# Performance work log

Measured on AMD Instinct MI355X. Metric: run time of the kernel, lower is better.

The kernel has to match this reference:

```python
import jax, jax.numpy as jnp
import numpy as np
from jax import lax

HIDDEN = 512
EPS = 1e-5


def _conv(x, w):
    # NCHW conv, 3x3, SAME padding, no bias (padding = kernel_size // 2 == 1)
    return lax.conv_general_dilated(
        x, w, window_strides=(1, 1), padding='SAME',
        dimension_numbers=('NCHW', 'OIHW', 'NCHW'))


def setup_inputs() -> dict:
    key = jax.random.key(0)
    ks = jax.random.split(key, 5)
    N, C, H, W = 32, HIDDEN, 32, 32
    fan = C * 9
    std = float(1.0 / np.sqrt(fan))
    return {
        'x': jax.random.normal(ks[0], (N, C, H, W), jnp.float32),
        'w_q': jax.random.normal(ks[1], (C, C, 3, 3), jnp.float32) * std,
        'w_k': jax.random.normal(ks[2], (C, C, 3, 3), jnp.float32) * std,
        'w_v': jax.random.normal(ks[3], (C, C, 3, 3), jnp.float32) * std,
        'w_o': jax.random.normal(ks[4], (C, C, 3, 3), jnp.float32) * std,
        'gamma': jnp.ones((C,), jnp.float32),
        'beta': jnp.zeros((C,), jnp.float32),
    }


def reference(x, w_q, w_k, w_v, w_o, gamma, beta):
    C = x.shape[1]
    q = _conv(x, w_q)  # [N,C,H,W]
    k = _conv(x, w_k)
    v = _conv(x, w_v)
    # (query.unsqueeze(1) * key.unsqueeze(0)).sum(2) == channel contraction
    att = jnp.einsum('ichw,jchw->ijhw', q, k) / jnp.sqrt(jnp.asarray(C, x.dtype))
    att = jax.nn.softmax(att, axis=1)  # softmax over key instances
    virt = jnp.einsum('ijhw,jchw->ichw', att, v)  # [N,C,H,W]
    # GroupNorm(1, C): normalize over (C,H,W) per instance, per-channel affine
    mean = jnp.mean(virt, axis=(1, 2, 3), keepdims=True)
    var = jnp.var(virt, axis=(1, 2, 3), keepdims=True)
    virt = (virt - mean) * lax.rsqrt(var + EPS)
    virt = virt * gamma[None, :, None, None] + beta[None, :, None, None]
    virt = jax.nn.relu(virt)
    virt = _conv(virt, w_o)
    # Dropout(0.2) is identity in eval mode
    return x + virt
```

## Files before the change

kernel.cpp:

```cpp
#include <hip/hip_runtime.h>

namespace {

constexpr int kN  = 32;
constexpr int kC  = 512;
constexpr int kH  = 32;
constexpr int kW  = 32;
constexpr int kHW = kH * kW;

constexpr int PCH   = 36992;
constexpr size_t WTF_ELEMS = (size_t)9 * kC * kC;
constexpr size_t XH_ELEMS  = (size_t)kN * 16 * PCH;
constexpr size_t QKV_ELEMS = (size_t)kN * kHW * kC;

using bf16x8 = __attribute__((ext_vector_type(8))) short;
using bf16x4 = __attribute__((ext_vector_type(4))) short;
using f32x4  = __attribute__((ext_vector_type(4))) float;

__device__ __forceinline__ float bf2f(short s) {
  unsigned u = ((unsigned)(unsigned short)s) << 16;
  return __builtin_bit_cast(float, u);
}
__device__ __forceinline__ short f2bf(float f) {
  unsigned u = __builtin_bit_cast(unsigned, f);
  u += 0x7FFFu + ((u >> 16) & 1u);
  return (short)(u >> 16);
}
__device__ __forceinline__ void gload_lds16(const void* g, void* l) {
  __builtin_amdgcn_global_load_lds(
      (const __attribute__((address_space(1))) void*)g,
      (__attribute__((address_space(3))) void*)l, 16, 0, 0);
}

__global__ __launch_bounds__(256) void wtf_pack_kernel(
    const float* __restrict__ wq, const float* __restrict__ wk,
    const float* __restrict__ wv, const float* __restrict__ wo,
    short* __restrict__ oq, short* __restrict__ ok,
    short* __restrict__ ov, short* __restrict__ oo) {
  const float* wsrc[4] = {wq, wk, wv, wo};
  short* wdst[4] = {oq, ok, ov, oo};
  const float* w = wsrc[blockIdx.z];
  short* wtf = wdst[blockIdx.z];
  __shared__ float tile[32][289];
  const int co0 = blockIdx.x * 32;
  const int ci0 = blockIdx.y * 32;
  for (int idx = threadIdx.x; idx < 32 * 288; idx += 256) {
    int c = idx % 288, r = idx / 288;
    tile[r][c] = w[(size_t)(co0 + r) * (kC * 9) + (size_t)ci0 * 9 + c];
  }
  __syncthreads();
  const int kkb  = ci0 >> 5;
  const int nnG0 = co0 >> 4;
  for (int g = threadIdx.x; g < 9 * 2 * 64; g += 256) {
    int laneg = g & 63;
    int nnL   = (g >> 6) & 1;
    int t     = g >> 7;
    int hi    = laneg >> 4;
    int coL   = nnL * 16 + (laneg & 15);
    bf16x8 pk;
#pragma unroll
    for (int j = 0; j < 8; ++j) pk[j] = f2bf(tile[coL][(hi * 8 + j) * 9 + t]);
    *(bf16x8*)&wtf[(((size_t)t * 16 + kkb) * 32 + nnG0 + nnL) * 512 + laneg * 8] = pk;
  }
}

__global__ __launch_bounds__(256) void x2xh_kernel(
    const float* __restrict__ x, short* __restrict__ xh) {
  __shared__ float tile[32][33];
  const int ch = blockIdx.x;
  const int h  = blockIdx.y;
  const int n  = blockIdx.z;
  const int w0 = threadIdx.x & 31;
  const int c0 = threadIdx.x >> 5;
#pragma unroll
  for (int pass = 0; pass < 4; ++pass) {
    int cir = pass * 8 + c0;
    tile[w0][cir] = x[(((size_t)n * kC + ch * 32 + cir) * kH + h) * kW + w0];
  }
  __syncthreads();
  const int wv = threadIdx.x >> 3;
  const int g4 = (threadIdx.x & 7) * 4;
  bf16x4 pk;
#pragma unroll
  for (int j = 0; j < 4; ++j) pk[j] = f2bf(tile[wv][g4 + j]);
  *(bf16x4*)&xh[(((size_t)n * 16 + ch) * 1156 + (size_t)(h + 1) * 34 + (wv + 1)) * 32 + g4] = pk;
}

__global__ __launch_bounds__(256) void halo_zero_kernel(
    short* __restrict__ xh, short* __restrict__ vh) {
  short* base = (blockIdx.x & 1) ? vh : xh;
  const int plane = blockIdx.x >> 1;
  short* dst = base + (size_t)plane * PCH;
  const int t = threadIdx.x;
  if (t < 132) {
    int row, col;
    if (t < 34)       { row = 0;          col = t; }
    else if (t < 68)  { row = 33;         col = t - 34; }
    else if (t < 100) { row = t - 68 + 1; col = 0; }
    else              { row = t - 100 + 1; col = 33; }
    const bf16x8 z = {0, 0, 0, 0, 0, 0, 0, 0};
    short* q = dst + (size_t)(row * 34 + col) * 32;
#pragma unroll
    for (int j = 0; j < 4; ++j) *(bf16x8*)&q[j * 8] = z;
  }
}

__global__ __launch_bounds__(256, 3) void conv_qkv_kernel(
    const short* __restrict__ xin,
    const short* __restrict__ wtq, const short* __restrict__ wtk,
    const short* __restrict__ wtv,
    short* __restrict__ outq, short* __restrict__ outk,
    short* __restrict__ outv) {
  __shared__ __align__(16) short As[3][8192];
  const int tid  = threadIdx.x;
  const int lane = tid & 63;
  const int l15  = lane & 15, lhi = lane >> 4;
  const int w    = tid >> 6;
  const int wbase = tid & 192;

  const int xcd = blockIdx.x & 7;
  const int m   = blockIdx.x >> 3;
  const int co0 = (m >> 5) * 64;
  const int spt = m & 7;
  const int n   = xcd * 4 + ((m >> 3) & 3);
  const int h0  = spt * 4;
  const int sp0 = spt * 128;

  const short* srcA = xin + (size_t)n * (16 * PCH) + (size_t)h0 * (34 * 32);
  const size_t boff = ((size_t)(co0 >> 4) + w) * 512 + lane * 8;
  const short* bp[3] = {wtq + boff, wtk + boff, wtv + boff};

  f32x4 acc[3][8];
#pragma unroll
  for (int c = 0; c < 3; ++c)
#pragma unroll
    for (int mf = 0; mf < 8; ++mf)
#pragma unroll
      for (int r = 0; r < 4; ++r) acc[c][mf][r] = 0.f;

#define STAGE_A(kk, buf)                                                      \
  {                                                                           \
    const short* gA = srcA + (size_t)(kk) * PCH;                              \
    _Pragma("unroll") for (int pass = 0; pass < 4; ++pass)                    \
        gload_lds16(gA + (size_t)(pass * 256 + tid) * 8,                      \
                    &As[buf][(pass * 256 + wbase) * 8]);                      \
  }

  STAGE_A(0, 0);
  STAGE_A(1, 1);
  bf16x8 cur[3];
#pragma unroll
  for (int j = 0; j < 3; ++j)
    cur[j] = *(const bf16x8*)&bp[j][0];

  int ab = 0;
  int sb = 2;
  for (int kk = 0; kk < 16; ++kk) {
    asm volatile("s_waitcnt vmcnt(7)" ::: "memory");
    __builtin_amdgcn_s_barrier();
#pragma unroll
    for (int t = 0; t < 9; ++t) {
      if (t == 1 && kk < 14) STAGE_A(kk + 2, sb);
      const int dy = t / 3, dx = t % 3;
      bf16x8 a[8];
#pragma unroll
      for (int mf = 0; mf < 8; ++mf) {
        const int pb = ((mf >> 1) + dy) * 34 + (mf & 1) * 16 + l15 + dx;
        a[mf] = *(const bf16x8*)&As[ab][pb * 32 + lhi * 8];
      }
      const int nt  = (t < 8) ? (t + 1) : 0;
      const int nkk = (t < 8) ? kk : kk + 1;
      const size_t bo = (size_t)(nt * 16 + nkk) * 16384;
#pragma unroll
      for (int c = 0; c < 3; ++c) {
        __builtin_amdgcn_s_setprio(1);
#pragma unroll
        for (int mf = 0; mf < 8; ++mf)
          acc[c][mf] = __builtin_amdgcn_mfma_f32_16x16x32_bf16(
              a[mf], cur[c], acc[c][mf], 0, 0, 0);
        __builtin_amdgcn_s_setprio(0);
        cur[c] = *(const bf16x8*)&bp[c][bo];
      }
    }
    ab = (ab == 2) ? 0 : ab + 1;
    sb = (sb == 2) ? 0 : sb + 1;
  }
#undef STAGE_A

  short* outs[3] = {outq, outk, outv};
#pragma unroll
  for (int c = 0; c < 3; ++c) {
    short* out = outs[c];
#pragma unroll
    for (int mf = 0; mf < 8; ++mf)
#pragma unroll
      for (int r = 0; r < 4; ++r) {
        size_t off = ((size_t)n * kHW + sp0 + mf * 16 + lhi * 4 + r) * kC
                     + co0 + w * 16 + l15;
        out[off] = f2bf(acc[c][mf][r]);
      }
  }
}

__global__ __launch_bounds__(256, 3) void conv_o_kernel(
    const short* __restrict__ xin, const short* __restrict__ wtf,
    const float* __restrict__ xres, float* __restrict__ out) {
  __shared__ __align__(16) short As[3][8192];
  const int tid  = threadIdx.x;
  const int lane = tid & 63;
  const int l15  = lane & 15, lhi = lane >> 4;
  const int w    = tid >> 6;
  const int wbase = tid & 192;

  const int xcd = blockIdx.x & 7;
  const int m   = blockIdx.x >> 3;
  const int co0 = (m >> 5) * 128;
  const int spt = m & 7;
  const int n   = xcd * 4 + ((m >> 3) & 3);
  const int h0  = spt * 4;
  const int sp0 = spt * 128;

  const short* srcA = xin + (size_t)n * (16 * PCH) + (size_t)h0 * (34 * 32);
  const short* bptr = wtf + ((size_t)(co0 >> 4) + w * 2) * 512 + lane * 8;

  f32x4 acc[2][8];
#pragma unroll
  for (int nf = 0; nf < 2; ++nf)
#pragma unroll
    for (int mf = 0; mf < 8; ++mf)
#pragma unroll
      for (int r = 0; r < 4; ++r) acc[nf][mf][r] = 0.f;

#define STAGE_A(kk, buf)                                                      \
  {                                                                           \
    const short* gA = srcA + (size_t)(kk) * PCH;                              \
    _Pragma("unroll") for (int pass = 0; pass < 4; ++pass)                    \
        gload_lds16(gA + (size_t)(pass * 256 + tid) * 8,                      \
                    &As[buf][(pass * 256 + wbase) * 8]);                      \
  }

  STAGE_A(0, 0);
  STAGE_A(1, 1);
  bf16x8 cur[2], nxt[2];
#pragma unroll
  for (int j = 0; j < 2; ++j)
    cur[j] = *(const bf16x8*)&bptr[(size_t)j * 512];

  int ab = 0, sb = 2;
  for (int kk = 0; kk < 16; ++kk) {
    asm volatile("s_waitcnt vmcnt(6)" ::: "memory");
    __builtin_amdgcn_s_barrier();
#pragma unroll
    for (int t = 0; t < 9; ++t) {
      {
        const int nt  = (t < 8) ? (t + 1) : 0;
        const int nkk = (t < 8) ? kk : kk + 1;
        const size_t bo = (size_t)(nt * 16 + nkk) * 16384;
#pragma unroll
        for (int j = 0; j < 2; ++j)
          nxt[j] = *(const bf16x8*)&bptr[bo + (size_t)j * 512];
      }
      if (t == 1 && kk < 14) STAGE_A(kk + 2, sb);
      const int dy = t / 3, dx = t % 3;
      bf16x8 a[8];
#pragma unroll
      for (int mf = 0; mf < 8; ++mf) {
        const int pb = ((mf >> 1) + dy) * 34 + (mf & 1) * 16 + l15 + dx;
        a[mf] = *(const bf16x8*)&As[ab][pb * 32 + lhi * 8];
      }
      __builtin_amdgcn_s_setprio(1);
#pragma unroll
      for (int nf = 0; nf < 2; ++nf)
#pragma unroll
        for (int mf = 0; mf < 8; ++mf)
          acc[nf][mf] = __builtin_amdgcn_mfma_f32_16x16x32_bf16(
              a[mf], cur[nf], acc[nf][mf], 0, 0, 0);
      __builtin_amdgcn_s_setprio(0);
#pragma unroll
      for (int j = 0; j < 2; ++j) cur[j] = nxt[j];
    }
    ab = (ab == 2) ? 0 : ab + 1;
    sb = (sb == 2) ? 0 : sb + 1;
  }
#undef STAGE_A

  float* T = (float*)&As[0][0];
#pragma unroll
  for (int nf = 0; nf < 2; ++nf) {
    __syncthreads();
    const int tr = w * 16 + l15;
#pragma unroll
    for (int mf = 0; mf < 8; ++mf)
#pragma unroll
      for (int r = 0; r < 4; ++r)
        T[tr * 129 + mf * 16 + lhi * 4 + r] = acc[nf][mf][r];
    __syncthreads();
#pragma unroll
    for (int it = 0; it < 32; ++it) {
      int idx = it * 256 + tid;
      int trr = idx >> 7, sp = idx & 127;
      int co = co0 + (trr >> 4) * 32 + nf * 16 + (trr & 15);
      size_t off = ((size_t)n * kC + co) * kHW + sp0 + sp;
      out[off] = T[trr * 129 + sp] + xres[off];
    }
  }
}

__global__ __launch_bounds__(256) void attn_mfma_kernel(
    const short* q, const short* __restrict__ k,
    const short* __restrict__ v, short* virt, float* __restrict__ gsum) {
  __shared__ __align__(16) short Qs[32 * 72];
  __shared__ __align__(16) short Ks[32 * 72];
  __shared__ __align__(16) float Ps[32 * 36];
  __shared__ __align__(16) short Vt[64 * 40];
  const int p    = blockIdx.x;
  const int tid  = threadIdx.x;
  const int lane = tid & 63;
  const int l15  = lane & 15, lhi = lane >> 4;
  const int w    = tid >> 6;
  const int iq   = w >> 1, jq = w & 1;

  f32x4 accS = {0.f, 0.f, 0.f, 0.f};
  const int si = tid >> 3;
  const int sc = (tid & 7) * 8;
  for (int c0 = 0; c0 < kC; c0 += 64) {
    __syncthreads();
    {
      size_t g = ((size_t)si * kHW + p) * kC + c0 + sc;
      *(bf16x8*)&Qs[si * 72 + sc] = *(const bf16x8*)&q[g];
      *(bf16x8*)&Ks[si * 72 + sc] = *(const bf16x8*)&k[g];
    }
    __syncthreads();
#pragma unroll
    for (int cs = 0; cs < 2; ++cs) {
      bf16x8 aq = *(const bf16x8*)&Qs[(iq * 16 + l15) * 72 + cs * 32 + lhi * 8];
      bf16x8 bk = *(const bf16x8*)&Ks[(jq * 16 + l15) * 72 + cs * 32 + lhi * 8];
      accS = __builtin_amdgcn_mfma_f32_16x16x32_bf16(aq, bk, accS, 0, 0, 0);
    }
  }
  __syncthreads();
  constexpr float scale = 0.044194173824159216f;
#pragma unroll
  for (int r = 0; r < 4; ++r)
    Ps[(iq * 16 + lhi * 4 + r) * 36 + jq * 16 + l15] = accS[r] * scale;
  __syncthreads();

  {
    const int i  = tid >> 3;
    const int j0 = (tid & 7) * 4;
    float a0 = Ps[i * 36 + j0], a1 = Ps[i * 36 + j0 + 1];
    float a2 = Ps[i * 36 + j0 + 2], a3 = Ps[i * 36 + j0 + 3];
    float mx = fmaxf(fmaxf(a0, a1), fmaxf(a2, a3));
    for (int off = 1; off < 8; off <<= 1) mx = fmaxf(mx, __shfl_xor(mx, off));
    float e0 = __expf(a0 - mx), e1 = __expf(a1 - mx);
    float e2 = __expf(a2 - mx), e3 = __expf(a3 - mx);
    float s = e0 + e1 + e2 + e3;
    for (int off = 1; off < 8; off <<= 1) s += __shfl_xor(s, off);
    const float inv = 1.f / s;
    Ps[i * 36 + j0]     = e0 * inv;
    Ps[i * 36 + j0 + 1] = e1 * inv;
    Ps[i * 36 + j0 + 2] = e2 * inv;
    Ps[i * 36 + j0 + 3] = e3 * inv;
  }
  __syncthreads();

  bf16x8 ap[2];
#pragma unroll
  for (int it = 0; it < 2; ++it) {
    const float* pr = &Ps[(it * 16 + l15) * 36 + lhi * 8];
    float4 lo = *(const float4*)pr;
    float4 hi4 = *(const float4*)(pr + 4);
    ap[it][0] = f2bf(lo.x);  ap[it][1] = f2bf(lo.y);
    ap[it][2] = f2bf(lo.z);  ap[it][3] = f2bf(lo.w);
    ap[it][4] = f2bf(hi4.x); ap[it][5] = f2bf(hi4.y);
    ap[it][6] = f2bf(hi4.z); ap[it][7] = f2bf(hi4.w);
  }
  __syncthreads();

  float gs[8], gq2[8];
#pragma unroll
  for (int idx = 0; idx < 8; ++idx) { gs[idx] = 0.f; gq2[idx] = 0.f; }

  const f32x4 zacc = {0.f, 0.f, 0.f, 0.f};
  for (int c0 = 0; c0 < kC; c0 += 64) {
    __syncthreads();
    {
      const int j = tid >> 3, c8g = tid & 7;
      bf16x8 vvv = *(const bf16x8*)&v[((size_t)j * kHW + p) * kC + c0 + c8g * 8];
#pragma unroll
      for (int jj = 0; jj < 8; ++jj) {
        int c = c8g * 8 + jj;
        int byte = (c * 80 + j * 2) ^ (((c >> 3) & 7) << 4);
        *(short*)((char*)Vt + byte) = vvv[jj];
      }
    }
    __syncthreads();
    {
      const int c = w * 16 + l15;
      const int byte = (c * 80 + lhi * 16) ^ (((c >> 3) & 7) << 4);
      bf16x8 bv = *(const bf16x8*)((const char*)Vt + byte);
#pragma unroll
      for (int it = 0; it < 2; ++it) {
        f32x4 o = __builtin_amdgcn_mfma_f32_16x16x32_bf16(ap[it], bv, zacc, 0, 0, 0);
#pragma unroll
        for (int r = 0; r < 4; ++r) {
          short ob = f2bf(o[r]);
          virt[((size_t)(it * 16 + lhi * 4 + r) * kHW + p) * kC + c0 + w * 16 + l15] = ob;
          float fv = bf2f(ob);
          gs[it * 4 + r] += fv;
          gq2[it * 4 + r] = fmaf(fv, fv, gq2[it * 4 + r]);
        }
      }
    }
  }

#pragma unroll
  for (int idx = 0; idx < 8; ++idx)
    for (int off = 1; off < 16; off <<= 1) {
      gs[idx]  += __shfl_xor(gs[idx], off);
      gq2[idx] += __shfl_xor(gq2[idx], off);
    }
  __syncthreads();
  float* SS = Ps;
  if (l15 == 0) {
#pragma unroll
    for (int idx = 0; idx < 8; ++idx) {
      int it = idx >> 2, r = idx & 3;
      int i = it * 16 + lhi * 4 + r;
      SS[(w * 32 + i) * 2]     = gs[idx];
      SS[(w * 32 + i) * 2 + 1] = gq2[idx];
    }
  }
  __syncthreads();
  if (tid < 32) {
    float s = 0.f, q2 = 0.f;
#pragma unroll
    for (int ww = 0; ww < 4; ++ww) {
      s  += SS[(ww * 32 + tid) * 2];
      q2 += SS[(ww * 32 + tid) * 2 + 1];
    }
    atomicAdd(&gsum[tid], s);
    atomicAdd(&gsum[32 + tid], q2);
  }
}

__global__ __launch_bounds__(64) void gn_final_kernel(
    const float* __restrict__ gsum, float* __restrict__ stats) {
  if (threadIdx.x < 32) {
    constexpr float invn = 1.f / ((float)kHW * kC);
    float mean = gsum[threadIdx.x] * invn;
    float var = gsum[32 + threadIdx.x] * invn - mean * mean;
    stats[threadIdx.x] = mean;
    stats[32 + threadIdx.x] = rsqrtf(var + 1e-5f);
  }
}

__global__ __launch_bounds__(256) void gn_apply_kernel(
    const short* __restrict__ virt, const float* __restrict__ stats,
    const float* __restrict__ gamma, const float* __restrict__ beta,
    short* __restrict__ vh) {
  const size_t g = (size_t)blockIdx.x * 256 + threadIdx.x;
  const int i    = (int)(g >> 16);
  const int rest = (int)(g & 65535);
  const int p    = rest >> 6;
  const int c8g  = rest & 63;
  const int ci   = c8g * 8;
  const float mean = stats[i];
  const float rstd = stats[32 + i];
  bf16x8 vv = *(const bf16x8*)&virt[((size_t)i * kHW + p) * kC + ci];
  const float4 ga = ((const float4*)gamma)[c8g * 2];
  const float4 gb = ((const float4*)gamma)[c8g * 2 + 1];
  const float4 ba = ((const float4*)beta)[c8g * 2];
  const float4 bb = ((const float4*)beta)[c8g * 2 + 1];
  const float gv[8] = {ga.x, ga.y, ga.z, ga.w, gb.x, gb.y, gb.z, gb.w};
  const float bv[8] = {ba.x, ba.y, ba.z, ba.w, bb.x, bb.y, bb.z, bb.w};
  bf16x8 o;
#pragma unroll
  for (int jj = 0; jj < 8; ++jj) {
    float f = (bf2f(vv[jj]) - mean) * rstd;
    f = fmaxf(fmaf(f, gv[jj], bv[jj]), 0.f);
    o[jj] = f2bf(f);
  }
  const size_t dst =
      (((size_t)i * 16 + (ci >> 5)) * 1156 + (size_t)((p >> 5) + 1) * 34 + (p & 31) + 1) * 32
      + (ci & 31);
  *(bf16x8*)&vh[dst] = o;
}

}

extern "C" void kernel_launch(void* const* d_in, const int* in_sizes, int n_in,
                              void* d_out, int out_size, void* d_ws,
                              size_t ws_size, hipStream_t stream) {
  const float* x     = (const float*)d_in[0];
  const float* w_q   = (const float*)d_in[1];
  const float* w_k   = (const float*)d_in[2];
  const float* w_v   = (const float*)d_in[3];
  const float* w_o   = (const float*)d_in[4];
  const float* gamma = (const float*)d_in[5];
  const float* beta  = (const float*)d_in[6];

  short* ws    = (short*)d_ws;
  short* wtf_q = ws;
  short* wtf_k = wtf_q + WTF_ELEMS;
  short* wtf_v = wtf_k + WTF_ELEMS;
  short* wtf_o = wtf_v + WTF_ELEMS;
  short* xh    = wtf_o + WTF_ELEMS;
  short* vh    = xh + XH_ELEMS;
  short* qb    = vh + XH_ELEMS;
  short* kb    = qb + QKV_ELEMS;
  short* vb    = kb + QKV_ELEMS;
  float* stats = (float*)(vb + QKV_ELEMS);
  float* gsum  = stats + 64;
  short* virt  = qb;
  halo_zero_kernel<<<1024, 256, 0, stream>>>(xh, vh);
  hipMemsetAsync(gsum, 0, 64 * sizeof(float), stream);

  wtf_pack_kernel<<<dim3(16, 16, 4), 256, 0, stream>>>(
      w_q, w_k, w_v, w_o, wtf_q, wtf_k, wtf_v, wtf_o);

  x2xh_kernel<<<dim3(16, 32, 32), 256, 0, stream>>>(x, xh);

  conv_qkv_kernel<<<2048, 256, 0, stream>>>(xh, wtf_q, wtf_k, wtf_v,
                                            qb, kb, vb);

  attn_mfma_kernel<<<kHW, 256, 0, stream>>>(qb, kb, vb, virt, gsum);

  gn_final_kernel<<<1, 64, 0, stream>>>(gsum, stats);
  gn_apply_kernel<<<(int)(QKV_ELEMS / 8 / 256), 256, 0, stream>>>(
      virt, stats, gamma, beta, vh);

  conv_o_kernel<<<1024, 256, 0, stream>>>(vh, wtf_o, x, (float*)d_out);
}
```

Measured before the change: 553.3 us.

## Interleave QKV weights and double-buffer attention LDS tiles with register prefetch

The packed Q/K/V conv weights now sit interleaved in one buffer, so each wave's three weight fragments for a tap are adjacent in memory and come from one base pointer, which should improve locality and reduce address arithmetic. The attention kernel double-buffers its Q/K and V LDS tiles and prefetches the next channel slice into registers while the current slice is consumed. This removes one barrier per loop iteration and hides global load latency, at the cost of extra LDS and register use.

```diff
diff --git a/kernel.cpp b/kernel.cpp
--- a/kernel.cpp
+++ b/kernel.cpp
@@ -35,12 +35,10 @@
 __global__ __launch_bounds__(256) void wtf_pack_kernel(
     const float* __restrict__ wq, const float* __restrict__ wk,
     const float* __restrict__ wv, const float* __restrict__ wo,
-    short* __restrict__ oq, short* __restrict__ ok,
-    short* __restrict__ ov, short* __restrict__ oo) {
+    short* __restrict__ wqkv, short* __restrict__ wo_out) {
   const float* wsrc[4] = {wq, wk, wv, wo};
-  short* wdst[4] = {oq, ok, ov, oo};
-  const float* w = wsrc[blockIdx.z];
-  short* wtf = wdst[blockIdx.z];
+  const int z = blockIdx.z;
+  const float* w = wsrc[z];
   __shared__ float tile[32][289];
   const int co0 = blockIdx.x * 32;
   const int ci0 = blockIdx.y * 32;
@@ -60,7 +58,13 @@
     bf16x8 pk;
 #pragma unroll
     for (int j = 0; j < 8; ++j) pk[j] = f2bf(tile[coL][(hi * 8 + j) * 9 + t]);
-    *(bf16x8*)&wtf[(((size_t)t * 16 + kkb) * 32 + nnG0 + nnL) * 512 + laneg * 8] = pk;
+    if (z < 3) {
+      *(bf16x8*)&wqkv[((((size_t)t * 16 + kkb) * 32 + nnG0 + nnL) * 3 + z) * 512
+                      + laneg * 8] = pk;
+    } else {
+      *(bf16x8*)&wo_out[(((size_t)t * 16 + kkb) * 32 + nnG0 + nnL) * 512
+                        + laneg * 8] = pk;
+    }
   }
 }
 
@@ -106,9 +110,7 @@
 }
 
 __global__ __launch_bounds__(256, 3) void conv_qkv_kernel(
-    const short* __restrict__ xin,
-    const short* __restrict__ wtq, const short* __restrict__ wtk,
-    const short* __restrict__ wtv,
+    const short* __restrict__ xin, const short* __restrict__ wqkv,
     short* __restrict__ outq, short* __restrict__ outk,
     short* __restrict__ outv) {
   __shared__ __align__(16) short As[3][8192];
@@ -127,8 +129,7 @@
   const int sp0 = spt * 128;
 
   const short* srcA = xin + (size_t)n * (16 * PCH) + (size_t)h0 * (34 * 32);
-  const size_t boff = ((size_t)(co0 >> 4) + w) * 512 + lane * 8;
-  const short* bp[3] = {wtq + boff, wtk + boff, wtv + boff};
+  const short* bbase = wqkv + ((size_t)(co0 >> 4) + w) * 1536 + lane * 8;
 
   f32x4 acc[3][8];
 #pragma unroll
@@ -151,7 +152,7 @@
   bf16x8 cur[3];
 #pragma unroll
   for (int j = 0; j < 3; ++j)
-    cur[j] = *(const bf16x8*)&bp[j][0];
+    cur[j] = *(const bf16x8*)&bbase[(size_t)j * 512];
 
   int ab = 0;
   int sb = 2;
@@ -170,7 +171,8 @@
       }
       const int nt  = (t < 8) ? (t + 1) : 0;
       const int nkk = (t < 8) ? kk : kk + 1;
-      const size_t bo = (size_t)(nt * 16 + nkk) * 16384;
+      const size_t bo = (size_t)(nt * 16 + nkk) * 49152;
+      const short* brel = &bbase[bo];
 #pragma unroll
       for (int c = 0; c < 3; ++c) {
         __builtin_amdgcn_s_setprio(1);
@@ -179,7 +181,7 @@
           acc[c][mf] = __builtin_amdgcn_mfma_f32_16x16x32_bf16(
               a[mf], cur[c], acc[c][mf], 0, 0, 0);
         __builtin_amdgcn_s_setprio(0);
-        cur[c] = *(const bf16x8*)&bp[c][bo];
+        cur[c] = *(const bf16x8*)&brel[(size_t)c * 512];
       }
     }
     ab = (ab == 2) ? 0 : ab + 1;
@@ -309,10 +311,10 @@
 __global__ __launch_bounds__(256) void attn_mfma_kernel(
     const short* q, const short* __restrict__ k,
     const short* __restrict__ v, short* virt, float* __restrict__ gsum) {
-  __shared__ __align__(16) short Qs[32 * 72];
-  __shared__ __align__(16) short Ks[32 * 72];
+  __shared__ __align__(16) short Qs[2][32 * 72];
+  __shared__ __align__(16) short Ks[2][32 * 72];
   __shared__ __align__(16) float Ps[32 * 36];
-  __shared__ __align__(16) short Vt[64 * 40];
+  __shared__ __align__(16) short Vt[2][64 * 40];
   const int p    = blockIdx.x;
   const int tid  = threadIdx.x;
   const int lane = tid & 63;
@@ -323,18 +325,22 @@
   f32x4 accS = {0.f, 0.f, 0.f, 0.f};
   const int si = tid >> 3;
   const int sc = (tid & 7) * 8;
-  for (int c0 = 0; c0 < kC; c0 += 64) {
+  const size_t gstep = ((size_t)si * kHW + p) * kC + sc;
+  bf16x8 rq = *(const bf16x8*)&q[gstep];
+  bf16x8 rk = *(const bf16x8*)&k[gstep];
+  for (int i = 0; i < 8; ++i) {
+    const int cb = i & 1;
+    *(bf16x8*)&Qs[cb][si * 72 + sc] = rq;
+    *(bf16x8*)&Ks[cb][si * 72 + sc] = rk;
+    if (i < 7) {
+      rq = *(const bf16x8*)&q[gstep + (i + 1) * 64];
+      rk = *(const bf16x8*)&k[gstep + (i + 1) * 64];
+    }
     __syncthreads();
-    {
-      size_t g = ((size_t)si * kHW + p) * kC + c0 + sc;
-      *(bf16x8*)&Qs[si * 72 + sc] = *(const bf16x8*)&q[g];
-      *(bf16x8*)&Ks[si * 72 + sc] = *(const bf16x8*)&k[g];
-    }
-    __syncthreads();
 #pragma unroll
     for (int cs = 0; cs < 2; ++cs) {
-      bf16x8 aq = *(const bf16x8*)&Qs[(iq * 16 + l15) * 72 + cs * 32 + lhi * 8];
-      bf16x8 bk = *(const bf16x8*)&Ks[(jq * 16 + l15) * 72 + cs * 32 + lhi * 8];
+      bf16x8 aq = *(const bf16x8*)&Qs[cb][(iq * 16 + l15) * 72 + cs * 32 + lhi * 8];
+      bf16x8 bk = *(const bf16x8*)&Ks[cb][(jq * 16 + l15) * 72 + cs * 32 + lhi * 8];
       accS = __builtin_amdgcn_mfma_f32_16x16x32_bf16(aq, bk, accS, 0, 0, 0);
     }
   }
@@ -382,23 +388,27 @@
   for (int idx = 0; idx < 8; ++idx) { gs[idx] = 0.f; gq2[idx] = 0.f; }
 
   const f32x4 zacc = {0.f, 0.f, 0.f, 0.f};
-  for (int c0 = 0; c0 < kC; c0 += 64) {
+  const int vj = tid >> 3, vc8 = tid & 7;
+  const size_t vstep = ((size_t)vj * kHW + p) * kC + vc8 * 8;
+  bf16x8 rv = *(const bf16x8*)&v[vstep];
+  for (int i = 0; i < 8; ++i) {
+    const int cb = i & 1;
+    {
+      char* vtb = (char*)&Vt[cb][0];
+#pragma unroll
+      for (int jj = 0; jj < 8; ++jj) {
+        int c = vc8 * 8 + jj;
+        int byte = (c * 80 + vj * 2) ^ (((c >> 3) & 7) << 4);
+        *(short*)(vtb + byte) = rv[jj];
+      }
+    }
+    if (i < 7) rv = *(const bf16x8*)&v[vstep + (i + 1) * 64];
     __syncthreads();
     {
-      const int j = tid >> 3, c8g = tid & 7;
-      bf16x8 vvv = *(const bf16x8*)&v[((size_t)j * kHW + p) * kC + c0 + c8g * 8];
-#pragma unroll
-      for (int jj = 0; jj < 8; ++jj) {
-        int c = c8g * 8 + jj;
-        int byte = (c * 80 + j * 2) ^ (((c >> 3) & 7) << 4);
-        *(short*)((char*)Vt + byte) = vvv[jj];
-      }
-    }
-    __syncthreads();
-    {
+      const int c0 = i * 64;
       const int c = w * 16 + l15;
       const int byte = (c * 80 + lhi * 16) ^ (((c >> 3) & 7) << 4);
-      bf16x8 bv = *(const bf16x8*)((const char*)Vt + byte);
+      bf16x8 bv = *(const bf16x8*)((const char*)&Vt[cb][0] + byte);
 #pragma unroll
       for (int it = 0; it < 2; ++it) {
         f32x4 o = __builtin_amdgcn_mfma_f32_16x16x32_bf16(ap[it], bv, zacc, 0, 0, 0);
@@ -501,10 +511,8 @@
   const float* beta  = (const float*)d_in[6];
 
   short* ws    = (short*)d_ws;
-  short* wtf_q = ws;
-  short* wtf_k = wtf_q + WTF_ELEMS;
-  short* wtf_v = wtf_k + WTF_ELEMS;
-  short* wtf_o = wtf_v + WTF_ELEMS;
+  short* wqkv  = ws;
+  short* wtf_o = wqkv + 3 * WTF_ELEMS;
   short* xh    = wtf_o + WTF_ELEMS;
   short* vh    = xh + XH_ELEMS;
   short* qb    = vh + XH_ELEMS;
@@ -517,12 +525,11 @@
   hipMemsetAsync(gsum, 0, 64 * sizeof(float), stream);
 
   wtf_pack_kernel<<<dim3(16, 16, 4), 256, 0, stream>>>(
-      w_q, w_k, w_v, w_o, wtf_q, wtf_k, wtf_v, wtf_o);
+      w_q, w_k, w_v, w_o, wqkv, wtf_o);
 
   x2xh_kernel<<<dim3(16, 32, 32), 256, 0, stream>>>(x, xh);
 
-  conv_qkv_kernel<<<2048, 256, 0, stream>>>(xh, wtf_q, wtf_k, wtf_v,
-                                            qb, kb, vb);
+  conv_qkv_kernel<<<2048, 256, 0, stream>>>(xh, wqkv, qb, kb, vb);
 
   attn_mfma_kernel<<<kHW, 256, 0, stream>>>(qb, kb, vb, virt, gsum);
 
```

New measurement: 544.0 us. No clear change (-1.7%).
